# Kernel tuning notes

Measured on AMD Instinct MI355X. Metric: run time of the kernel, lower is better.

## Reference

```python
import jax, jax.numpy as jnp
import numpy as np

BS, RES = 2, 512
H_LVL = RES // 2 + 1   # floor(512/2)+1 = 257
W_LVL = RES            # 512
NQ = H_LVL * W_LVL     # 131584
D, HEADS, PTS = 128, 8, 4
DH = D // HEADS


def setup_inputs() -> dict:
    key = jax.random.key(0)
    ks = jax.random.split(key, 9)
    s = 0.02  # weight init scale
    return {
        "query":   jax.random.normal(ks[0], (BS, NQ, D), jnp.float32),
        "W_value": jax.random.normal(ks[1], (D, D), jnp.float32) * s,
        "b_value": jax.random.normal(ks[2], (D,), jnp.float32) * s,
        "W_off":   jax.random.normal(ks[3], (D, HEADS * PTS * 2), jnp.float32) * s,
        "b_off":   jax.random.normal(ks[4], (HEADS * PTS * 2,), jnp.float32) * s,
        "W_attn":  jax.random.normal(ks[5], (D, HEADS * PTS), jnp.float32) * s,
        "b_attn":  jax.random.normal(ks[6], (HEADS * PTS,), jnp.float32) * s,
        "W_out":   jax.random.normal(ks[7], (D, D), jnp.float32) * s,
        "b_out":   jax.random.normal(ks[8], (D,), jnp.float32) * s,
    }


def _bilinear_zeros(V, x, y, H, W):
    """grid_sample(mode=bilinear, padding=zeros, align_corners=False) equivalent.
    V: [G, H*W, DH]; x, y: [G, S] pixel coords. Returns [G, S, DH]."""
    x0 = jnp.floor(x); y0 = jnp.floor(y)
    x0i = x0.astype(jnp.int32); y0i = y0.astype(jnp.int32)
    x1i = x0i + 1; y1i = y0i + 1
    wx1 = x - x0; wx0 = 1.0 - wx1
    wy1 = y - y0; wy0 = 1.0 - wy1

    def corner(xi, yi, w):
        valid = (xi >= 0) & (xi < W) & (yi >= 0) & (yi < H)
        idx = jnp.clip(yi, 0, H - 1) * W + jnp.clip(xi, 0, W - 1)
        val = jnp.take_along_axis(V, idx[:, :, None], axis=1)  # [G,S,DH]
        return (w * valid.astype(w.dtype))[:, :, None] * val

    return (corner(x0i, y0i, wx0 * wy0) + corner(x1i, y0i, wx1 * wy0)
            + corner(x0i, y1i, wx0 * wy1) + corner(x1i, y1i, wx1 * wy1))


def reference(query, W_value, b_value, W_off, b_off, W_attn, b_attn, W_out, b_out):
    B, NQ_, D_ = query.shape
    H, W = H_LVL, W_LVL

    # projections (mmcv MSDeformAttn)
    value = (query @ W_value + b_value).reshape(B, NQ_, HEADS, DH)
    offsets = (query @ W_off + b_off).reshape(B, NQ_, HEADS, PTS, 2)  # num_levels=1
    attn = jax.nn.softmax((query @ W_attn + b_attn).reshape(B, NQ_, HEADS, PTS), axis=-1)

    # reference points: meshgrid of normalized (col=x, row=y), row-major flatten
    gy, gx = jnp.meshgrid(jnp.linspace(0.0, 1.0, H), jnp.linspace(0.0, 1.0, W), indexing="ij")
    ref = jnp.stack([gx, gy], axis=-1).reshape(NQ_, 2).astype(query.dtype)  # [NQ,2]

    # sampling locations in [0,1]; offset normalizer = (W, H)
    norm = jnp.array([W, H], dtype=query.dtype)
    loc = ref[None, :, None, None, :] + offsets / norm  # [B,NQ,HEADS,PTS,2]

    # grid_sample align_corners=False: pixel = loc*size - 0.5
    x = loc[..., 0] * W - 0.5
    y = loc[..., 1] * H - 0.5

    G = B * HEADS
    V = value.transpose(0, 2, 1, 3).reshape(G, H * W, DH)          # [G,HW,DH]
    xs = x.transpose(0, 2, 1, 3).reshape(G, NQ_ * PTS)
    ys = y.transpose(0, 2, 1, 3).reshape(G, NQ_ * PTS)

    samp = _bilinear_zeros(V, xs, ys, H, W).reshape(B, HEADS, NQ_, PTS, DH)
    aw = attn.transpose(0, 2, 1, 3)                                 # [B,HEADS,NQ,PTS]
    out = jnp.einsum("bhqp,bhqpd->bqhd", aw, samp).reshape(B, NQ_, D_)
    out = out @ W_out + b_out

    # mmcv adds identity inside the attention module; outer forward adds residual again
    return out + query + query
```

## Files before the change

### kernel.cpp

```cpp
#include <hip/hip_runtime.h>
#include <hip/hip_bf16.h>

#define BS     2
#define H_LVL  257
#define W_LVL  512
#define NQC    (H_LVL * W_LVL)
#define DD     128
#define HEADS  8
#define PTS    4
#define DH     16
#define MTOT   (BS * NQC)

typedef float v4f __attribute__((ext_vector_type(4)));
typedef short v8s __attribute__((ext_vector_type(8)));

static __device__ __forceinline__ unsigned short f2bb(float f) {
    union { float f; unsigned int u; } v; v.f = f;
    const unsigned int u = v.u;
    return (unsigned short)((u + 0x7fffu + ((u >> 16) & 1u)) >> 16);
}
static __device__ __forceinline__ float bb2f(unsigned short h) {
    union { unsigned int u; float f; } v; v.u = ((unsigned int)h) << 16;
    return v.f;
}
static __device__ __forceinline__ void fma4(float4& acc, float w, const unsigned short* p) {
    const ushort4 r = *(const ushort4*)p;
    acc.x = fmaf(w, bb2f(r.x), acc.x);
    acc.y = fmaf(w, bb2f(r.y), acc.y);
    acc.z = fmaf(w, bb2f(r.z), acc.z);
    acc.w = fmaf(w, bb2f(r.w), acc.w);
}

__global__ __launch_bounds__(256) void prep_kernel(
    const float* __restrict__ Wv, const float* __restrict__ bv,
    const float* __restrict__ Woff, const float* __restrict__ boff,
    const float* __restrict__ Wattn, const float* __restrict__ battn,
    const float* __restrict__ Wout,
    unsigned short* __restrict__ Wt224, unsigned short* __restrict__ WtO,
    float* __restrict__ bcat224)
{
    const int id = blockIdx.x * 256 + threadIdx.x;
    {
        const int n = id >> 7, k = id & 127;
        float v;
        if (n < 128)      v = Wv[k * DD + n];
        else if (n < 192) v = Woff[k * 64 + (n - 128)];
        else              v = Wattn[k * 32 + (n - 192)];
        Wt224[id] = f2bb(v);
    }
    if (id < 128 * 128) {
        const int n = id >> 7, k = id & 127;
        WtO[id] = f2bb(Wout[k * DD + n]);
    }
    if (id < 224)
        bcat224[id] = (id < 128) ? bv[id] : (id < 192 ? boff[id - 128] : battn[id - 192]);
}

__global__ __launch_bounds__(256) void gemm_fused_kernel(
    const float* __restrict__ A,
    const unsigned short* __restrict__ Wt,
    const float* __restrict__ bias,
    unsigned short* __restrict__ value,
    unsigned short* __restrict__ proj)
{
    constexpr int NT = 14;
    constexpr int NC = NT * 16;
    __shared__ unsigned short As[64 * 136];
    __shared__ unsigned short Ws[NC * 136];
    const int t = threadIdx.x;
    const long long m0 = (long long)blockIdx.x * 64;

    {
        const float4* src = (const float4*)(A + m0 * DD);
        #pragma unroll
        for (int rep = 0; rep < 8; ++rep) {
            const int c = rep * 256 + t;
            const int m = c >> 5, f4 = c & 31;
            const float4 v = src[c];
            ushort4 hq;
            hq.x = f2bb(v.x); hq.y = f2bb(v.y); hq.z = f2bb(v.z); hq.w = f2bb(v.w);
            *(ushort4*)(&As[m * 136 + f4 * 4]) = hq;
        }
    }
    {
        const uint4* src = (const uint4*)Wt;
        #pragma unroll
        for (int rep = 0; rep < 14; ++rep) {
            const int c = rep * 256 + t;
            const int n = c >> 4, kc = c & 15;
            *(uint4*)(&Ws[n * 136 + kc * 8]) = src[c];
        }
    }
    __syncthreads();

    const int lane = t & 63, wave = t >> 6;
    const int l15 = lane & 15, quad = lane >> 4;

    v4f acc[NT];
    #pragma unroll
    for (int nt = 0; nt < NT; ++nt) { v4f z = {0.f, 0.f, 0.f, 0.f}; acc[nt] = z; }

    const int arow = wave * 16 + l15;
    #pragma unroll
    for (int kk = 0; kk < 4; ++kk) {
        const v8s a = *(const v8s*)(&As[arow * 136 + kk * 32 + quad * 8]);
        #pragma unroll
        for (int nt = 0; nt < NT; ++nt) {
            const v8s b = *(const v8s*)(&Ws[(nt * 16 + l15) * 136 + kk * 32 + quad * 8]);
            acc[nt] = __builtin_amdgcn_mfma_f32_16x16x32_bf16(a, b, acc[nt], 0, 0, 0);
        }
    }

    const long long mbase = m0 + wave * 16 + quad * 4;
    const int b = (int)(m0 / NQC);
    #pragma unroll
    for (int nt = 0; nt < 8; ++nt) {
        const float bi = bias[nt * 16 + l15];
        #pragma unroll
        for (int r = 0; r < 4; ++r) {
            const long long q = (mbase + r) - (long long)b * NQC;
            value[((long long)(b * HEADS + nt) * NQC + q) * DH + l15] =
                f2bb(acc[nt][r] + bi);
        }
    }
    #pragma unroll
    for (int nt = 8; nt < 14; ++nt) {
        const float bi = bias[nt * 16 + l15];
        #pragma unroll
        for (int r = 0; r < 4; ++r)
            proj[(mbase + r) * 96 + (nt - 8) * 16 + l15] = f2bb(acc[nt][r] + bi);
    }
}

template<int NT, int MODE>
__global__ __launch_bounds__(256) void gemm_kernel(
    const float* __restrict__ A,
    const unsigned short* __restrict__ Wt,
    const float* __restrict__ bias,
    unsigned short* __restrict__ dst_bf,
    float* __restrict__ dst_f,
    const float* __restrict__ query)
{
    constexpr int NC = NT * 16;
    __shared__ unsigned short As[64 * 136];
    __shared__ unsigned short Ws[NC * 136];
    const int t = threadIdx.x;
    const long long m0 = (long long)blockIdx.x * 64;

    {
        const float4* src = (const float4*)(A + m0 * DD);
        #pragma unroll
        for (int rep = 0; rep < 8; ++rep) {
            const int c = rep * 256 + t;
            const int m = c >> 5, f4 = c & 31;
            const float4 v = src[c];
            ushort4 hq;
            hq.x = f2bb(v.x); hq.y = f2bb(v.y); hq.z = f2bb(v.z); hq.w = f2bb(v.w);
            *(ushort4*)(&As[m * 136 + f4 * 4]) = hq;
        }
    }
    {
        const uint4* src = (const uint4*)Wt;
        for (int c = t; c < NC * 16; c += 256) {
            const int n = c >> 4, kc = c & 15;
            *(uint4*)(&Ws[n * 136 + kc * 8]) = src[c];
        }
    }
    __syncthreads();

    const int lane = t & 63, wave = t >> 6;
    const int l15 = lane & 15, quad = lane >> 4;

    v4f acc[NT];
    #pragma unroll
    for (int nt = 0; nt < NT; ++nt) { v4f z = {0.f, 0.f, 0.f, 0.f}; acc[nt] = z; }

    const int arow = wave * 16 + l15;
    #pragma unroll
    for (int kk = 0; kk < 4; ++kk) {
        const v8s a = *(const v8s*)(&As[arow * 136 + kk * 32 + quad * 8]);
        #pragma unroll
        for (int nt = 0; nt < NT; ++nt) {
            const v8s b = *(const v8s*)(&Ws[(nt * 16 + l15) * 136 + kk * 32 + quad * 8]);
            acc[nt] = __builtin_amdgcn_mfma_f32_16x16x32_bf16(a, b, acc[nt], 0, 0, 0);
        }
    }

    const long long mbase = m0 + wave * 16 + quad * 4;
    if (MODE == 0) {
        const int b = (int)(m0 / NQC);
        #pragma unroll
        for (int nt = 0; nt < NT; ++nt) {
            const float bi = bias[nt * 16 + l15];
            #pragma unroll
            for (int r = 0; r < 4; ++r) {
                const long long q = (mbase + r) - (long long)b * NQC;
                dst_bf[((long long)(b * HEADS + nt) * NQC + q) * DH + l15] =
                    f2bb(acc[nt][r] + bi);
            }
        }
    } else {
        #pragma unroll
        for (int nt = 0; nt < NT; ++nt) {
            const float bi = bias[nt * 16 + l15];
            #pragma unroll
            for (int r = 0; r < 4; ++r) {
                const long long idx = (mbase + r) * DD + nt * 16 + l15;
                dst_f[idx] = acc[nt][r] + bi + 2.0f * query[idx];
            }
        }
    }
}

__global__ __launch_bounds__(256) void gemm_out_kernel(
    const unsigned short* Abf,
    const unsigned short* __restrict__ Wt,
    const float* __restrict__ bias,
    float* dst,
    const float* __restrict__ query)
{
    constexpr int NT = 8;
    __shared__ unsigned short As[64 * 136];
    __shared__ unsigned short Ws[128 * 136];
    const int t = threadIdx.x;
    const long long m0 = (long long)blockIdx.x * 64;

    {
        const uint4* src = (const uint4*)((const char*)Abf + ((size_t)blockIdx.x << 15));
        #pragma unroll
        for (int rep = 0; rep < 4; ++rep) {
            const int c = rep * 256 + t;
            const int m = c >> 4, kc = c & 15;
            *(uint4*)(&As[m * 136 + kc * 8]) = src[c];
        }
    }
    {
        const uint4* src = (const uint4*)Wt;
        #pragma unroll
        for (int rep = 0; rep < 8; ++rep) {
            const int c = rep * 256 + t;
            const int n = c >> 4, kc = c & 15;
            *(uint4*)(&Ws[n * 136 + kc * 8]) = src[c];
        }
    }
    __syncthreads();

    const int lane = t & 63, wave = t >> 6;
    const int l15 = lane & 15, quad = lane >> 4;

    v4f acc[NT];
    #pragma unroll
    for (int nt = 0; nt < NT; ++nt) { v4f z = {0.f, 0.f, 0.f, 0.f}; acc[nt] = z; }

    const int arow = wave * 16 + l15;
    #pragma unroll
    for (int kk = 0; kk < 4; ++kk) {
        const v8s a = *(const v8s*)(&As[arow * 136 + kk * 32 + quad * 8]);
        #pragma unroll
        for (int nt = 0; nt < NT; ++nt) {
            const v8s b = *(const v8s*)(&Ws[(nt * 16 + l15) * 136 + kk * 32 + quad * 8]);
            acc[nt] = __builtin_amdgcn_mfma_f32_16x16x32_bf16(a, b, acc[nt], 0, 0, 0);
        }
    }

    const long long mbase = m0 + wave * 16 + quad * 4;
    #pragma unroll
    for (int nt = 0; nt < NT; ++nt) {
        const float bi = bias[nt * 16 + l15];
        #pragma unroll
        for (int r = 0; r < 4; ++r) {
            const long long idx = (mbase + r) * DD + nt * 16 + l15;
            dst[idx] = acc[nt][r] + bi + 2.0f * query[idx];
        }
    }
}

template<bool PRECOMP, bool BF16OUT>
__global__ __launch_bounds__(256) void sample2_kernel(
    const unsigned short* __restrict__ proj,
    const float* __restrict__ query,
    const float* __restrict__ Woff, const float* __restrict__ boff,
    const float* __restrict__ Wattn, const float* __restrict__ battn,
    const unsigned short* __restrict__ value,
    float* __restrict__ attn_out)
{
    __shared__ float projF[8][96];
    const int t = threadIdx.x;
    const long long qbase = (long long)blockIdx.x * 8;

    if constexpr (PRECOMP) {
        if (t < 192) {
            const ushort4 r = *(const ushort4*)(proj + qbase * 96 + t * 4);
            const int qq = (t * 4) / 96, c = (t * 4) % 96;
            projF[qq][c]     = bb2f(r.x);
            projF[qq][c + 1] = bb2f(r.y);
            projF[qq][c + 2] = bb2f(r.z);
            projF[qq][c + 3] = bb2f(r.w);
        }
        __syncthreads();
    } else {
        __shared__ float qs[8][DD];
        {
            const int qi = t >> 5, k4 = (t & 31) * 4;
            const float4 v = *(const float4*)(query + (qbase + qi) * DD + k4);
            qs[qi][k4] = v.x; qs[qi][k4 + 1] = v.y; qs[qi][k4 + 2] = v.z; qs[qi][k4 + 3] = v.w;
        }
        __syncthreads();
        for (int task = t; task < 768; task += 256) {
            const int qi = task / 96, c = task % 96;
            float a; const float* wp; int stride;
            if (c < 64) { a = boff[c];       wp = Woff  + c;        stride = 64; }
            else        { a = battn[c - 64]; wp = Wattn + (c - 64); stride = 32; }
            for (int k = 0; k < DD; ++k) a += qs[qi][k] * wp[k * stride];
            projF[qi][c] = a;
        }
        __syncthreads();
    }

    const int q_loc = t >> 5, lq = t & 31;
    const int h = lq >> 2, p_own = lq & 3;
    const long long bq = qbase + q_loc;
    const int b = (int)(bq / NQC);
    const int qidx = (int)(bq - (long long)b * NQC);
    const int row = qidx >> 9, col = qidx & 511;

    const float offx = projF[q_loc][(h * PTS + p_own) * 2];
    const float offy = projF[q_loc][(h * PTS + p_own) * 2 + 1];
    const float al   = projF[q_loc][64 + h * PTS + p_own];
    float mx = fmaxf(al, __shfl_xor(al, 1));
    mx = fmaxf(mx, __shfl_xor(mx, 2));
    const float e = __expf(al - mx);
    float sm = e + __shfl_xor(e, 1);
    sm += __shfl_xor(sm, 2);
    const float aw = e / sm;

    const float x = (float)col * (1.0f / 511.0f) * (float)W_LVL + offx - 0.5f;
    const float y = (float)row * (1.0f / 256.0f) * (float)H_LVL + offy - 0.5f;
    const float x0f = floorf(x), y0f = floorf(y);
    const int x0 = (int)x0f, y0 = (int)y0f;
    const int x1 = x0 + 1, y1 = y0 + 1;
    const float wx1 = x - x0f, wx0 = 1.0f - wx1;
    const float wy1 = y - y0f, wy0 = 1.0f - wy1;
    const float vx0 = (x0 >= 0 && x0 < W_LVL) ? 1.f : 0.f;
    const float vx1 = (x1 >= 0 && x1 < W_LVL) ? 1.f : 0.f;
    const float vy0 = (y0 >= 0 && y0 < H_LVL) ? 1.f : 0.f;
    const float vy1 = (y1 >= 0 && y1 < H_LVL) ? 1.f : 0.f;
    float w00 = aw * wx0 * wy0 * vx0 * vy0;
    float w01 = aw * wx1 * wy0 * vx1 * vy0;
    float w10 = aw * wx0 * wy1 * vx0 * vy1;
    float w11 = aw * wx1 * wy1 * vx1 * vy1;
    const int xc0 = min(max(x0, 0), W_LVL - 1), xc1 = min(max(x1, 0), W_LVL - 1);
    const int yc0 = min(max(y0, 0), H_LVL - 1), yc1 = min(max(y1, 0), H_LVL - 1);
    int i00 = yc0 * W_LVL + xc0, i01 = yc0 * W_LVL + xc1;
    int i10 = yc1 * W_LVL + xc0, i11 = yc1 * W_LVL + xc1;

    const int dq4 = p_own;
    const unsigned short* V = value + (size_t)(b * HEADS + h) * NQC * DH + dq4 * 4;
    float4 acc = {0.f, 0.f, 0.f, 0.f};
    const int lbase = (t & 63) & ~3;
    #pragma unroll
    for (int p = 0; p < 4; ++p) {
        const int src = lbase + p;
        const float W00 = __shfl(w00, src, 64), W01 = __shfl(w01, src, 64);
        const float W10 = __shfl(w10, src, 64), W11 = __shfl(w11, src, 64);
        const int   I00 = __shfl(i00, src, 64), I01 = __shfl(i01, src, 64);
        const int   I10 = __shfl(i10, src, 64), I11 = __shfl(i11, src, 64);
        fma4(acc, W00, V + (size_t)I00 * DH);
        fma4(acc, W01, V + (size_t)I01 * DH);
        fma4(acc, W10, V + (size_t)I10 * DH);
        fma4(acc, W11, V + (size_t)I11 * DH);
    }
    if constexpr (BF16OUT) {
        ushort4 h4;
        h4.x = f2bb(acc.x); h4.y = f2bb(acc.y); h4.z = f2bb(acc.z); h4.w = f2bb(acc.w);
        char* dstp = (char*)attn_out + (((size_t)(bq >> 6)) << 15)
                   + (((size_t)(bq & 63)) << 8) + (size_t)(h * 32 + dq4 * 8);
        *(ushort4*)dstp = h4;
    } else {
        *(float4*)(attn_out + bq * DD + h * DH + dq4 * 4) = acc;
    }
}

extern "C" void kernel_launch(void* const* d_in, const int* in_sizes, int n_in,
                              void* d_out, int out_size, void* d_ws, size_t ws_size,
                              hipStream_t stream) {
    const float* query = (const float*)d_in[0];
    const float* Wv    = (const float*)d_in[1];
    const float* bv    = (const float*)d_in[2];
    const float* Woff  = (const float*)d_in[3];
    const float* boff  = (const float*)d_in[4];
    const float* Wattn = (const float*)d_in[5];
    const float* battn = (const float*)d_in[6];
    const float* Wout  = (const float*)d_in[7];
    const float* bout  = (const float*)d_in[8];
    float* out = (float*)d_out;

    char* ws = (char*)d_ws;
    size_t off = 0;
    unsigned short* Wt224 = (unsigned short*)(ws + off); off += 224 * 128 * 2;
    unsigned short* WtO   = (unsigned short*)(ws + off); off += 128 * 128 * 2;
    float*          bcat  = (float*)(ws + off);          off += 224 * 4;
    off = (off + 255) & ~(size_t)255;
    unsigned short* value = (unsigned short*)(ws + off);
    off += (size_t)BS * HEADS * NQC * DH * 2;
    off = (off + 255) & ~(size_t)255;
    unsigned short* proj = (unsigned short*)(ws + off);
    const size_t proj_need = (size_t)MTOT * 96 * 2;
    const bool precomp = (ws_size >= off + proj_need);

    prep_kernel<<<112, 256, 0, stream>>>(Wv, bv, Woff, boff, Wattn, battn, Wout,
                                         Wt224, WtO, bcat);
    if (precomp) {
        gemm_fused_kernel<<<MTOT / 64, 256, 0, stream>>>(query, Wt224, bcat, value, proj);
        sample2_kernel<true, true><<<MTOT / 8, 256, 0, stream>>>(
            proj, nullptr, nullptr, nullptr, nullptr, nullptr, value, out);
        gemm_out_kernel<<<MTOT / 64, 256, 0, stream>>>(
            (const unsigned short*)out, WtO, bout, out, query);
    } else {
        gemm_kernel<8, 0><<<MTOT / 64, 256, 0, stream>>>(query, Wt224, bcat, value,
                                                         nullptr, nullptr);
        sample2_kernel<false, false><<<MTOT / 8, 256, 0, stream>>>(
            nullptr, query, Woff, boff, Wattn, battn, value, out);
        gemm_kernel<8, 2><<<MTOT / 64, 256, 0, stream>>>(out, WtO, bout, nullptr, out, query);
    }
}
```

Measured before the change: 387.1 us.

## Fuse deformable sampling with output projection GEMM in one kernel

Merges the bilinear sampling kernel and the output projection GEMM into one kernel that handles 64 queries per block. The sampled bf16 attention output stays in shared memory as the GEMM A-tile instead of being written to and reread from global memory. One kernel launch is also removed. In exchange, each block uses more LDS (a projF/Ws union plus As), which may lower occupancy for the latency-bound gather phase. The sampling also becomes a serialized 8-iteration loop per block.

New measurement: 398.9 us. +3.0%, slower.

```diff
diff --git a/kernel.cpp b/kernel.cpp
--- a/kernel.cpp
+++ b/kernel.cpp
@@ -212,35 +212,106 @@
     }
 }
 
-__global__ __launch_bounds__(256) void gemm_out_kernel(
-    const unsigned short* Abf,
-    const unsigned short* __restrict__ Wt,
-    const float* __restrict__ bias,
-    float* dst,
-    const float* __restrict__ query)
+__global__ __launch_bounds__(256) void sample_out_kernel(
+    const unsigned short* __restrict__ proj,
+    const unsigned short* __restrict__ value,
+    const unsigned short* __restrict__ WtO,
+    const float* __restrict__ bout,
+    const float* __restrict__ query,
+    float* __restrict__ out)
 {
-    constexpr int NT = 8;
+    __shared__ union {
+        float projF[64][96];
+        unsigned short Ws[128 * 136];
+    } sh;
     __shared__ unsigned short As[64 * 136];
-    __shared__ unsigned short Ws[128 * 136];
+
     const int t = threadIdx.x;
-    const long long m0 = (long long)blockIdx.x * 64;
-
-    {
-        const uint4* src = (const uint4*)((const char*)Abf + ((size_t)blockIdx.x << 15));
-        #pragma unroll
-        for (int rep = 0; rep < 4; ++rep) {
-            const int c = rep * 256 + t;
-            const int m = c >> 4, kc = c & 15;
-            *(uint4*)(&As[m * 136 + kc * 8]) = src[c];
-        }
-    }
-    {
-        const uint4* src = (const uint4*)Wt;
+    const long long qbase = (long long)blockIdx.x * 64;
+
+    {
+        const ushort4* src = (const ushort4*)(proj + qbase * 96);
+        #pragma unroll
+        for (int rep = 0; rep < 6; ++rep) {
+            const int i = rep * 256 + t;
+            const ushort4 r = src[i];
+            const int qq = (i * 4) / 96, c = (i * 4) % 96;
+            sh.projF[qq][c]     = bb2f(r.x);
+            sh.projF[qq][c + 1] = bb2f(r.y);
+            sh.projF[qq][c + 2] = bb2f(r.z);
+            sh.projF[qq][c + 3] = bb2f(r.w);
+        }
+    }
+    __syncthreads();
+
+    const int b = (int)(qbase / NQC);
+    const int lq = t & 31;
+    const int h = lq >> 2, p_own = lq & 3;
+    const int lbase = (t & 63) & ~3;
+    const unsigned short* V = value + (size_t)(b * HEADS + h) * NQC * DH + p_own * 4;
+
+    #pragma unroll
+    for (int it = 0; it < 8; ++it) {
+        const int q_loc = it * 8 + (t >> 5);
+        const int qidx = (int)(qbase - (long long)b * NQC) + q_loc;
+        const int row = qidx >> 9, col = qidx & 511;
+
+        const float offx = sh.projF[q_loc][(h * PTS + p_own) * 2];
+        const float offy = sh.projF[q_loc][(h * PTS + p_own) * 2 + 1];
+        const float al   = sh.projF[q_loc][64 + h * PTS + p_own];
+        float mx = fmaxf(al, __shfl_xor(al, 1));
+        mx = fmaxf(mx, __shfl_xor(mx, 2));
+        const float e = __expf(al - mx);
+        float sm = e + __shfl_xor(e, 1);
+        sm += __shfl_xor(sm, 2);
+        const float aw = e / sm;
+
+        const float x = (float)col * (1.0f / 511.0f) * (float)W_LVL + offx - 0.5f;
+        const float y = (float)row * (1.0f / 256.0f) * (float)H_LVL + offy - 0.5f;
+        const float x0f = floorf(x), y0f = floorf(y);
+        const int x0 = (int)x0f, y0 = (int)y0f;
+        const int x1 = x0 + 1, y1 = y0 + 1;
+        const float wx1 = x - x0f, wx0 = 1.0f - wx1;
+        const float wy1 = y - y0f, wy0 = 1.0f - wy1;
+        const float vx0 = (x0 >= 0 && x0 < W_LVL) ? 1.f : 0.f;
+        const float vx1 = (x1 >= 0 && x1 < W_LVL) ? 1.f : 0.f;
+        const float vy0 = (y0 >= 0 && y0 < H_LVL) ? 1.f : 0.f;
+        const float vy1 = (y1 >= 0 && y1 < H_LVL) ? 1.f : 0.f;
+        float w00 = aw * wx0 * wy0 * vx0 * vy0;
+        float w01 = aw * wx1 * wy0 * vx1 * vy0;
+        float w10 = aw * wx0 * wy1 * vx0 * vy1;
+        float w11 = aw * wx1 * wy1 * vx1 * vy1;
+        const int xc0 = min(max(x0, 0), W_LVL - 1), xc1 = min(max(x1, 0), W_LVL - 1);
+        const int yc0 = min(max(y0, 0), H_LVL - 1), yc1 = min(max(y1, 0), H_LVL - 1);
+        int i00 = yc0 * W_LVL + xc0, i01 = yc0 * W_LVL + xc1;
+        int i10 = yc1 * W_LVL + xc0, i11 = yc1 * W_LVL + xc1;
+
+        float4 acc = {0.f, 0.f, 0.f, 0.f};
+        #pragma unroll
+        for (int p = 0; p < 4; ++p) {
+            const int src = lbase + p;
+            const float W00 = __shfl(w00, src, 64), W01 = __shfl(w01, src, 64);
+            const float W10 = __shfl(w10, src, 64), W11 = __shfl(w11, src, 64);
+            const int   I00 = __shfl(i00, src, 64), I01 = __shfl(i01, src, 64);
+            const int   I10 = __shfl(i10, src, 64), I11 = __shfl(i11, src, 64);
+            fma4(acc, W00, V + (size_t)I00 * DH);
+            fma4(acc, W01, V + (size_t)I01 * DH);
+            fma4(acc, W10, V + (size_t)I10 * DH);
+            fma4(acc, W11, V + (size_t)I11 * DH);
+        }
+        ushort4 h4;
+        h4.x = f2bb(acc.x); h4.y = f2bb(acc.y); h4.z = f2bb(acc.z); h4.w = f2bb(acc.w);
+        *(ushort4*)(&As[q_loc * 136 + h * 16 + p_own * 4]) = h4;
+    }
+    __syncthreads();
+
+    {
+        const uint4* src = (const uint4*)WtO;
         #pragma unroll
         for (int rep = 0; rep < 8; ++rep) {
             const int c = rep * 256 + t;
             const int n = c >> 4, kc = c & 15;
-            *(uint4*)(&Ws[n * 136 + kc * 8]) = src[c];
+            *(uint4*)(&sh.Ws[n * 136 + kc * 8]) = src[c];
         }
     }
     __syncthreads();
@@ -248,36 +319,34 @@
     const int lane = t & 63, wave = t >> 6;
     const int l15 = lane & 15, quad = lane >> 4;
 
-    v4f acc[NT];
-    #pragma unroll
-    for (int nt = 0; nt < NT; ++nt) { v4f z = {0.f, 0.f, 0.f, 0.f}; acc[nt] = z; }
+    v4f acc[8];
+    #pragma unroll
+    for (int nt = 0; nt < 8; ++nt) { v4f z = {0.f, 0.f, 0.f, 0.f}; acc[nt] = z; }
 
     const int arow = wave * 16 + l15;
     #pragma unroll
     for (int kk = 0; kk < 4; ++kk) {
         const v8s a = *(const v8s*)(&As[arow * 136 + kk * 32 + quad * 8]);
         #pragma unroll
-        for (int nt = 0; nt < NT; ++nt) {
-            const v8s b = *(const v8s*)(&Ws[(nt * 16 + l15) * 136 + kk * 32 + quad * 8]);
-            acc[nt] = __builtin_amdgcn_mfma_f32_16x16x32_bf16(a, b, acc[nt], 0, 0, 0);
-        }
-    }
-
-    const long long mbase = m0 + wave * 16 + quad * 4;
-    #pragma unroll
-    for (int nt = 0; nt < NT; ++nt) {
-        const float bi = bias[nt * 16 + l15];
+        for (int nt = 0; nt < 8; ++nt) {
+            const v8s bfr = *(const v8s*)(&sh.Ws[(nt * 16 + l15) * 136 + kk * 32 + quad * 8]);
+            acc[nt] = __builtin_amdgcn_mfma_f32_16x16x32_bf16(a, bfr, acc[nt], 0, 0, 0);
+        }
+    }
+
+    const long long mbase = qbase + wave * 16 + quad * 4;
+    #pragma unroll
+    for (int nt = 0; nt < 8; ++nt) {
+        const float bi = bout[nt * 16 + l15];
         #pragma unroll
         for (int r = 0; r < 4; ++r) {
             const long long idx = (mbase + r) * DD + nt * 16 + l15;
-            dst[idx] = acc[nt][r] + bi + 2.0f * query[idx];
-        }
-    }
-}
-
-template<bool PRECOMP, bool BF16OUT>
-__global__ __launch_bounds__(256) void sample2_kernel(
-    const unsigned short* __restrict__ proj,
+            out[idx] = acc[nt][r] + bi + 2.0f * query[idx];
+        }
+    }
+}
+
+__global__ __launch_bounds__(256) void sample2_fb_kernel(
     const float* __restrict__ query,
     const float* __restrict__ Woff, const float* __restrict__ boff,
     const float* __restrict__ Wattn, const float* __restrict__ battn,
@@ -288,34 +357,22 @@
     const int t = threadIdx.x;
     const long long qbase = (long long)blockIdx.x * 8;
 
-    if constexpr (PRECOMP) {
-        if (t < 192) {
-            const ushort4 r = *(const ushort4*)(proj + qbase * 96 + t * 4);
-            const int qq = (t * 4) / 96, c = (t * 4) % 96;
-            projF[qq][c]     = bb2f(r.x);
-            projF[qq][c + 1] = bb2f(r.y);
-            projF[qq][c + 2] = bb2f(r.z);
-            projF[qq][c + 3] = bb2f(r.w);
-        }
-        __syncthreads();
-    } else {
-        __shared__ float qs[8][DD];
-        {
-            const int qi = t >> 5, k4 = (t & 31) * 4;
-            const float4 v = *(const float4*)(query + (qbase + qi) * DD + k4);
-            qs[qi][k4] = v.x; qs[qi][k4 + 1] = v.y; qs[qi][k4 + 2] = v.z; qs[qi][k4 + 3] = v.w;
-        }
-        __syncthreads();
-        for (int task = t; task < 768; task += 256) {
-            const int qi = task / 96, c = task % 96;
-            float a; const float* wp; int stride;
-            if (c < 64) { a = boff[c];       wp = Woff  + c;        stride = 64; }
-            else        { a = battn[c - 64]; wp = Wattn + (c - 64); stride = 32; }
-            for (int k = 0; k < DD; ++k) a += qs[qi][k] * wp[k * stride];
-            projF[qi][c] = a;
-        }
-        __syncthreads();
-    }
+    __shared__ float qs[8][DD];
+    {
+        const int qi = t >> 5, k4 = (t & 31) * 4;
+        const float4 v = *(const float4*)(query + (qbase + qi) * DD + k4);
+        qs[qi][k4] = v.x; qs[qi][k4 + 1] = v.y; qs[qi][k4 + 2] = v.z; qs[qi][k4 + 3] = v.w;
+    }
+    __syncthreads();
+    for (int task = t; task < 768; task += 256) {
+        const int qi = task / 96, c = task % 96;
+        float a; const float* wp; int stride;
+        if (c < 64) { a = boff[c];       wp = Woff  + c;        stride = 64; }
+        else        { a = battn[c - 64]; wp = Wattn + (c - 64); stride = 32; }
+        for (int k = 0; k < DD; ++k) a += qs[qi][k] * wp[k * stride];
+        projF[qi][c] = a;
+    }
+    __syncthreads();
 
     const int q_loc = t >> 5, lq = t & 31;
     const int h = lq >> 2, p_own = lq & 3;
@@ -370,15 +427,7 @@
         fma4(acc, W10, V + (size_t)I10 * DH);
         fma4(acc, W11, V + (size_t)I11 * DH);
     }
-    if constexpr (BF16OUT) {
-        ushort4 h4;
-        h4.x = f2bb(acc.x); h4.y = f2bb(acc.y); h4.z = f2bb(acc.z); h4.w = f2bb(acc.w);
-        char* dstp = (char*)attn_out + (((size_t)(bq >> 6)) << 15)
-                   + (((size_t)(bq & 63)) << 8) + (size_t)(h * 32 + dq4 * 8);
-        *(ushort4*)dstp = h4;
-    } else {
-        *(float4*)(attn_out + bq * DD + h * DH + dq4 * 4) = acc;
-    }
+    *(float4*)(attn_out + bq * DD + h * DH + dq4 * 4) = acc;
 }
 
 extern "C" void kernel_launch(void* const* d_in, const int* in_sizes, int n_in,
@@ -412,15 +461,12 @@
                                          Wt224, WtO, bcat);
     if (precomp) {
         gemm_fused_kernel<<<MTOT / 64, 256, 0, stream>>>(query, Wt224, bcat, value, proj);
-        sample2_kernel<true, true><<<MTOT / 8, 256, 0, stream>>>(
-            proj, nullptr, nullptr, nullptr, nullptr, nullptr, value, out);
-        gemm_out_kernel<<<MTOT / 64, 256, 0, stream>>>(
-            (const unsigned short*)out, WtO, bout, out, query);
+        sample_out_kernel<<<MTOT / 64, 256, 0, stream>>>(proj, value, WtO, bout, query, out);
     } else {
         gemm_kernel<8, 0><<<MTOT / 64, 256, 0, stream>>>(query, Wt224, bcat, value,
                                                          nullptr, nullptr);
-        sample2_kernel<false, false><<<MTOT / 8, 256, 0, stream>>>(
-            nullptr, query, Woff, boff, Wattn, battn, value, out);
+        sample2_fb_kernel<<<MTOT / 8, 256, 0, stream>>>(query, Woff, boff,
+                                                        Wattn, battn, value, out);
         gemm_kernel<8, 2><<<MTOT / 64, 256, 0, stream>>>(out, WtO, bout, nullptr, out, query);
     }
 }
```
